# Kernel tuning notes

Hardware: AMD Instinct MI355X
Metric: run time of the kernel (lower is better)

Reference implementation:

```python
import jax, jax.numpy as jnp
import numpy as np

B, C, L = 8, 64, 65536  # batch, channels, flattened H*W
GN_EPS = 1e-5


def setup_inputs() -> dict:
    key = jax.random.key(0)
    ks = jax.random.split(key, 8)
    return {
        "x": jax.random.normal(ks[0], (B, C, L), dtype=jnp.float32),
        "inj0": jax.random.normal(ks[1], (B, C, L), dtype=jnp.float32),
        "inj1": jax.random.normal(ks[2], (B, C, L), dtype=jnp.float32),
        "residual": jax.random.normal(ks[3], (B, C, L), dtype=jnp.float32),
        "gate_w": jax.random.normal(ks[4], (C, C), dtype=jnp.float32) * (1.0 / np.sqrt(C)),
        "gate_b": jax.random.normal(ks[5], (C,), dtype=jnp.float32) * 0.01,
        "fuse_w": jax.random.normal(ks[6], (C, C), dtype=jnp.float32) * (1.0 / np.sqrt(C)),
        "fuse_b": jax.random.normal(ks[7], (C,), dtype=jnp.float32) * 0.01,
        "gn_w": jnp.ones((C,), dtype=jnp.float32),
        "gn_b": jnp.zeros((C,), dtype=jnp.float32),
    }


def _conv1x1(w, b, t):
    # Conv1d with kernel_size=1: [O,C] x [B,C,L] -> [B,O,L]
    return jnp.einsum('oc,bcl->bol', w, t) + b[None, :, None]


def reference(x, inj0, inj1, residual, gate_w, gate_b, fuse_w, fuse_b, gn_w, gn_b):
    # per-injection gate + elementwise multiply, summed over injections
    acc = jnp.zeros_like(x)
    for inj in (inj0, inj1):  # fixed small list of injection features
        acc = acc + x * _conv1x1(gate_w, gate_b, inj + x)
    # fuse conv + residual + ReLU (dropout p=0 -> identity)
    out = jax.nn.relu(_conv1x1(fuse_w, fuse_b, acc) + residual)
    # GroupNorm(num_groups=1): normalize over (C, L) per sample, per-channel affine
    mean = jnp.mean(out, axis=(1, 2), keepdims=True)
    var = jnp.var(out, axis=(1, 2), keepdims=True)
    out = (out - mean) * jax.lax.rsqrt(var + GN_EPS)
    return out * gn_w[None, :, None] + gn_b[None, :, None]
```

## Files before the change

### kernel.cpp

```cpp
#include <hip/hip_runtime.h>
#include <stdint.h>

#define Bv 8
#define Cv 64
#define Lv 65536
#define TPB 512
#define HALF 128
#define COLS 256
#define BLKS_PER_B (Lv / COLS)
#define GRID1 (Bv * BLKS_PER_B)


typedef __attribute__((ext_vector_type(8))) short short8;
typedef __attribute__((ext_vector_type(4))) float f32x4;

#define SSTRIDE 132

__device__ __forceinline__ uint16_t f2bf(float f) {
    uint32_t u = __float_as_uint(f);
    uint32_t r = u + 0x7FFFu + ((u >> 16) & 1u);
    return (uint16_t)(r >> 16);
}
__device__ __forceinline__ uint32_t pack2bf(float lo, float hi) {
    return (uint32_t)f2bf(lo) | ((uint32_t)f2bf(hi) << 16);
}

__global__ void pass1(const float* __restrict__ x, const float* __restrict__ inj0,
                      const float* __restrict__ inj1, const float* __restrict__ resid,
                      const float* __restrict__ gate_w, const float* __restrict__ gate_b,
                      const float* __restrict__ fuse_w, const float* __restrict__ fuse_b,
                      float* __restrict__ out, float* __restrict__ partials)
{
    __shared__ uint32_t s_buf[32 * SSTRIDE];
    __shared__ uint32_t w_lds[2][64][36];
    __shared__ float cinit[2][64];
    __shared__ float wred[16];

    const int tid  = threadIdx.x;
    const int lane = tid & 63;
    const int w    = tid >> 6;
    const int g    = lane >> 4;
    const int ln   = lane & 15;
    const int n    = 16 * w + ln;

    const int b    = blockIdx.x >> 8;
    const int lb   = blockIdx.x & 255;
    const int bCL  = b * (Cv * Lv);

    {
        const int mat = tid >> 8;
        const int m   = (tid >> 2) & 63;
        const int k0  = (tid & 3) << 4;
        const float* wsrc = mat ? fuse_w : gate_w;
        const float4* w4 = reinterpret_cast<const float4*>(wsrc + m * 64 + k0);
        uint32_t* dst = &w_lds[mat][m][k0 >> 1];
        #pragma unroll
        for (int q = 0; q < 4; ++q) {
            const float4 v = w4[q];
            dst[2 * q]     = pack2bf(v.x, v.y);
            dst[2 * q + 1] = pack2bf(v.z, v.w);
        }
        if (tid < 64) {
            cinit[0][tid] = 2.0f * gate_b[tid];
            cinit[1][tid] = fuse_b[tid];
        }
    }

    float lsum = 0.0f, lsq = 0.0f;

    #pragma unroll 1
    for (int h = 0; h < 2; ++h) {
        const int col0 = lb * COLS + h * HALF;

        #pragma unroll
        for (int uu = 0; uu < 2; ++uu) {
            const int u  = tid + uu * TPB;
            const int kp = u >> 5;
            const int c  = (u & 31) << 2;
            const int rA = bCL + (2 * kp) * Lv + col0 + c;
            const int rB = rA + Lv;
            const float4 xA = *reinterpret_cast<const float4*>(x    + rA);
            const float4 aA = *reinterpret_cast<const float4*>(inj0 + rA);
            const float4 bA = *reinterpret_cast<const float4*>(inj1 + rA);
            const float4 xB = *reinterpret_cast<const float4*>(x    + rB);
            const float4 aB = *reinterpret_cast<const float4*>(inj0 + rB);
            const float4 bB = *reinterpret_cast<const float4*>(inj1 + rB);
            uint4 dw;
            dw.x = pack2bf(aA.x + bA.x + 2.0f * xA.x, aB.x + bB.x + 2.0f * xB.x);
            dw.y = pack2bf(aA.y + bA.y + 2.0f * xA.y, aB.y + bB.y + 2.0f * xB.y);
            dw.z = pack2bf(aA.z + bA.z + 2.0f * xA.z, aB.z + bB.z + 2.0f * xB.z);
            dw.w = pack2bf(aA.w + bA.w + 2.0f * xA.w, aB.w + bB.w + 2.0f * xB.w);
            *reinterpret_cast<uint4*>(&s_buf[kp * SSTRIDE + c]) = dw;
        }
        __syncthreads();

        f32x4 D1[4];
        #pragma unroll
        for (int oc = 0; oc < 4; ++oc) {
            const float4 cb = *reinterpret_cast<const float4*>(&cinit[0][16 * oc + 4 * g]);
            D1[oc][0] = cb.x; D1[oc][1] = cb.y; D1[oc][2] = cb.z; D1[oc][3] = cb.w;
        }
        {
            uint4 B0, B1;
            B0.x = s_buf[(4 * g + 0) * SSTRIDE + n];
            B0.y = s_buf[(4 * g + 1) * SSTRIDE + n];
            B0.z = s_buf[(4 * g + 2) * SSTRIDE + n];
            B0.w = s_buf[(4 * g + 3) * SSTRIDE + n];
            B1.x = s_buf[(16 + 4 * g + 0) * SSTRIDE + n];
            B1.y = s_buf[(16 + 4 * g + 1) * SSTRIDE + n];
            B1.z = s_buf[(16 + 4 * g + 2) * SSTRIDE + n];
            B1.w = s_buf[(16 + 4 * g + 3) * SSTRIDE + n];
            #pragma unroll
            for (int oc = 0; oc < 4; ++oc) {
                const int m = ln + 16 * oc;
                const uint4 A0 = *reinterpret_cast<const uint4*>(&w_lds[0][m][4 * g]);
                const uint4 A1 = *reinterpret_cast<const uint4*>(&w_lds[0][m][16 + 4 * g]);
                D1[oc] = __builtin_amdgcn_mfma_f32_16x16x32_bf16(
                    __builtin_bit_cast(short8, A0), __builtin_bit_cast(short8, B0),
                    D1[oc], 0, 0, 0);
                D1[oc] = __builtin_amdgcn_mfma_f32_16x16x32_bf16(
                    __builtin_bit_cast(short8, A1), __builtin_bit_cast(short8, B1),
                    D1[oc], 0, 0, 0);
            }
        }

        {
            const int cg = bCL + col0 + n;
            #pragma unroll
            for (int oc = 0; oc < 4; ++oc) {
                const int m0 = 16 * oc + 4 * g;
                float av[4];
                #pragma unroll
                for (int j = 0; j < 4; ++j)
                    av[j] = x[cg + (m0 + j) * Lv] * D1[oc][j];
                const int kp = 8 * oc + 2 * g;
                s_buf[kp * SSTRIDE + n]       = pack2bf(av[0], av[1]);
                s_buf[(kp + 1) * SSTRIDE + n] = pack2bf(av[2], av[3]);
            }
        }
        __syncthreads();

        f32x4 D2[4];
        #pragma unroll
        for (int oc = 0; oc < 4; ++oc) {
            const float4 cb = *reinterpret_cast<const float4*>(&cinit[1][16 * oc + 4 * g]);
            D2[oc][0] = cb.x; D2[oc][1] = cb.y; D2[oc][2] = cb.z; D2[oc][3] = cb.w;
        }
        {
            uint4 B0, B1;
            B0.x = s_buf[(4 * g + 0) * SSTRIDE + n];
            B0.y = s_buf[(4 * g + 1) * SSTRIDE + n];
            B0.z = s_buf[(4 * g + 2) * SSTRIDE + n];
            B0.w = s_buf[(4 * g + 3) * SSTRIDE + n];
            B1.x = s_buf[(16 + 4 * g + 0) * SSTRIDE + n];
            B1.y = s_buf[(16 + 4 * g + 1) * SSTRIDE + n];
            B1.z = s_buf[(16 + 4 * g + 2) * SSTRIDE + n];
            B1.w = s_buf[(16 + 4 * g + 3) * SSTRIDE + n];
            #pragma unroll
            for (int oc = 0; oc < 4; ++oc) {
                const int m = ln + 16 * oc;
                const uint4 A0 = *reinterpret_cast<const uint4*>(&w_lds[1][m][4 * g]);
                const uint4 A1 = *reinterpret_cast<const uint4*>(&w_lds[1][m][16 + 4 * g]);
                D2[oc] = __builtin_amdgcn_mfma_f32_16x16x32_bf16(
                    __builtin_bit_cast(short8, A0), __builtin_bit_cast(short8, B0),
                    D2[oc], 0, 0, 0);
                D2[oc] = __builtin_amdgcn_mfma_f32_16x16x32_bf16(
                    __builtin_bit_cast(short8, A1), __builtin_bit_cast(short8, B1),
                    D2[oc], 0, 0, 0);
            }
        }
        __syncthreads();

        {
            float* uf = reinterpret_cast<float*>(s_buf);
            const int rowin = tid >> 4;
            const int cl    = tid & 15;
            #pragma unroll 1
            for (int ck = 0; ck < 2; ++ck) {
                #pragma unroll
                for (int oc2 = 0; oc2 < 2; ++oc2) {
                    const int oc = 2 * ck + oc2;
                    #pragma unroll
                    for (int j = 0; j < 4; ++j)
                        uf[(16 * oc2 + 4 * g + j) * SSTRIDE + n] = D2[oc][j];
                }
                const int m   = 32 * ck + rowin;
                const int gbm = bCL + m * Lv + col0;
                const float4 ra = *reinterpret_cast<const float4*>(&resid[gbm + 4 * cl]);
                const float4 rb = *reinterpret_cast<const float4*>(&resid[gbm + 4 * cl + 64]);
                __syncthreads();
                float4 va = *reinterpret_cast<const float4*>(&uf[rowin * SSTRIDE + 4 * cl]);
                float4 vb = *reinterpret_cast<const float4*>(&uf[rowin * SSTRIDE + 4 * cl + 64]);
                va.x = fmaxf(va.x + ra.x, 0.0f); va.y = fmaxf(va.y + ra.y, 0.0f);
                va.z = fmaxf(va.z + ra.z, 0.0f); va.w = fmaxf(va.w + ra.w, 0.0f);
                vb.x = fmaxf(vb.x + rb.x, 0.0f); vb.y = fmaxf(vb.y + rb.y, 0.0f);
                vb.z = fmaxf(vb.z + rb.z, 0.0f); vb.w = fmaxf(vb.w + rb.w, 0.0f);
                *reinterpret_cast<float4*>(&out[gbm + 4 * cl])      = va;
                *reinterpret_cast<float4*>(&out[gbm + 4 * cl + 64]) = vb;
                lsum += (va.x + va.y) + (va.z + va.w) + (vb.x + vb.y) + (vb.z + vb.w);
                lsq = fmaf(va.x, va.x, lsq); lsq = fmaf(va.y, va.y, lsq);
                lsq = fmaf(va.z, va.z, lsq); lsq = fmaf(va.w, va.w, lsq);
                lsq = fmaf(vb.x, vb.x, lsq); lsq = fmaf(vb.y, vb.y, lsq);
                lsq = fmaf(vb.z, vb.z, lsq); lsq = fmaf(vb.w, vb.w, lsq);
                __syncthreads();
            }
        }
    }

    #pragma unroll
    for (int st = 1; st < 64; st <<= 1) {
        lsum += __shfl_xor(lsum, st);
        lsq  += __shfl_xor(lsq,  st);
    }
    if (lane == 0) { wred[2 * w] = lsum; wred[2 * w + 1] = lsq; }
    __syncthreads();
    if (tid == 0) {
        float s = 0.0f, q = 0.0f;
        #pragma unroll
        for (int i = 0; i < 8; ++i) { s += wred[2 * i]; q += wred[2 * i + 1]; }
        partials[2 * blockIdx.x]     = s;
        partials[2 * blockIdx.x + 1] = q;
    }
}

__global__ __launch_bounds__(256)
void pass2(const float* __restrict__ partials, const float* __restrict__ gn_w,
           const float* __restrict__ gn_b, float* __restrict__ sb)
{
    __shared__ float r1[256], r2[256];
    __shared__ float mean_s, rs_s;
    const int b = blockIdx.x, tid = threadIdx.x;
    r1[tid] = partials[2 * (b * 256 + tid)];
    r2[tid] = partials[2 * (b * 256 + tid) + 1];
    __syncthreads();
    #pragma unroll
    for (int st = 128; st > 0; st >>= 1) {
        if (tid < st) { r1[tid] += r1[tid + st]; r2[tid] += r2[tid + st]; }
        __syncthreads();
    }
    if (tid == 0) {
        const float n = (float)Cv * (float)Lv;
        const float mean = r1[0] / n;
        const float var  = r2[0] / n - mean * mean;
        mean_s = mean;
        rs_s   = rsqrtf(var + 1e-5f);
    }
    __syncthreads();
    if (tid < Cv) {
        const float sc = gn_w[tid] * rs_s;
        sb[b * Cv + tid]           = sc;
        sb[Bv * Cv + b * Cv + tid] = fmaf(-mean_s, sc, gn_b[tid]);
    }
}

__global__ __launch_bounds__(256)
void pass3(float* __restrict__ out, const float* __restrict__ sb)
{
    const int total4 = (Bv * Cv * Lv) / 4;
    for (int i = blockIdx.x * blockDim.x + threadIdx.x; i < total4;
         i += gridDim.x * blockDim.x) {
        const int row = i >> 14;
        const float sc = sb[row];
        const float bi = sb[Bv * Cv + row];
        float4 v = reinterpret_cast<float4*>(out)[i];
        v.x = fmaf(v.x, sc, bi);
        v.y = fmaf(v.y, sc, bi);
        v.z = fmaf(v.z, sc, bi);
        v.w = fmaf(v.w, sc, bi);
        reinterpret_cast<float4*>(out)[i] = v;
    }
}

extern "C" void kernel_launch(void* const* d_in, const int* in_sizes, int n_in,
                              void* d_out, int out_size, void* d_ws, size_t ws_size,
                              hipStream_t stream)
{
    const float* x      = (const float*)d_in[0];
    const float* inj0   = (const float*)d_in[1];
    const float* inj1   = (const float*)d_in[2];
    const float* resid  = (const float*)d_in[3];
    const float* gate_w = (const float*)d_in[4];
    const float* gate_b = (const float*)d_in[5];
    const float* fuse_w = (const float*)d_in[6];
    const float* fuse_b = (const float*)d_in[7];
    const float* gn_w   = (const float*)d_in[8];
    const float* gn_b   = (const float*)d_in[9];

    float* out      = (float*)d_out;
    float* ws       = (float*)d_ws;
    float* partials = ws;
    float* sb       = ws + 2 * GRID1;

    hipLaunchKernelGGL(pass1, dim3(GRID1), dim3(TPB), 0, stream,
                       x, inj0, inj1, resid, gate_w, gate_b, fuse_w, fuse_b,
                       out, partials);
    hipLaunchKernelGGL(pass2, dim3(Bv), dim3(256), 0, stream,
                       partials, gn_w, gn_b, sb);
    hipLaunchKernelGGL(pass3, dim3(2048), dim3(256), 0, stream, out, sb);
}
```

Measured before the change: 191.4 us.

## Double-buffer staging LDS and prefetch next half-tile during GEMM

```diff
diff --git a/kernel.cpp b/kernel.cpp
--- a/kernel.cpp
+++ b/kernel.cpp
@@ -31,7 +31,7 @@
                       const float* __restrict__ fuse_w, const float* __restrict__ fuse_b,
                       float* __restrict__ out, float* __restrict__ partials)
 {
-    __shared__ uint32_t s_buf[32 * SSTRIDE];
+    __shared__ uint32_t s_buf[2][32 * SSTRIDE];
     __shared__ uint32_t w_lds[2][64][36];
     __shared__ float cinit[2][64];
     __shared__ float wred[16];
@@ -46,38 +46,15 @@
     const int b    = blockIdx.x >> 8;
     const int lb   = blockIdx.x & 255;
     const int bCL  = b * (Cv * Lv);
-
-    {
-        const int mat = tid >> 8;
-        const int m   = (tid >> 2) & 63;
-        const int k0  = (tid & 3) << 4;
-        const float* wsrc = mat ? fuse_w : gate_w;
-        const float4* w4 = reinterpret_cast<const float4*>(wsrc + m * 64 + k0);
-        uint32_t* dst = &w_lds[mat][m][k0 >> 1];
-        #pragma unroll
-        for (int q = 0; q < 4; ++q) {
-            const float4 v = w4[q];
-            dst[2 * q]     = pack2bf(v.x, v.y);
-            dst[2 * q + 1] = pack2bf(v.z, v.w);
-        }
-        if (tid < 64) {
-            cinit[0][tid] = 2.0f * gate_b[tid];
-            cinit[1][tid] = fuse_b[tid];
-        }
-    }
-
-    float lsum = 0.0f, lsq = 0.0f;
-
-    #pragma unroll 1
-    for (int h = 0; h < 2; ++h) {
-        const int col0 = lb * COLS + h * HALF;
-
+    const int tile0 = lb * COLS;
+
+    auto stage_half = [&](int dst, int scol) {
         #pragma unroll
         for (int uu = 0; uu < 2; ++uu) {
             const int u  = tid + uu * TPB;
             const int kp = u >> 5;
             const int c  = (u & 31) << 2;
-            const int rA = bCL + (2 * kp) * Lv + col0 + c;
+            const int rA = bCL + (2 * kp) * Lv + scol + c;
             const int rB = rA + Lv;
             const float4 xA = *reinterpret_cast<const float4*>(x    + rA);
             const float4 aA = *reinterpret_cast<const float4*>(inj0 + rA);
@@ -90,9 +67,47 @@
             dw.y = pack2bf(aA.y + bA.y + 2.0f * xA.y, aB.y + bB.y + 2.0f * xB.y);
             dw.z = pack2bf(aA.z + bA.z + 2.0f * xA.z, aB.z + bB.z + 2.0f * xB.z);
             dw.w = pack2bf(aA.w + bA.w + 2.0f * xA.w, aB.w + bB.w + 2.0f * xB.w);
-            *reinterpret_cast<uint4*>(&s_buf[kp * SSTRIDE + c]) = dw;
-        }
-        __syncthreads();
+            *reinterpret_cast<uint4*>(&s_buf[dst][kp * SSTRIDE + c]) = dw;
+        }
+    };
+
+    {
+        const int mat = tid >> 8;
+        const int m   = (tid >> 2) & 63;
+        const int k0  = (tid & 3) << 4;
+        const float* wsrc = mat ? fuse_w : gate_w;
+        const float4* w4 = reinterpret_cast<const float4*>(wsrc + m * 64 + k0);
+        uint32_t* dst = &w_lds[mat][m][k0 >> 1];
+        #pragma unroll
+        for (int q = 0; q < 4; ++q) {
+            const float4 v = w4[q];
+            dst[2 * q]     = pack2bf(v.x, v.y);
+            dst[2 * q + 1] = pack2bf(v.z, v.w);
+        }
+        if (tid < 64) {
+            cinit[0][tid] = 2.0f * gate_b[tid];
+            cinit[1][tid] = fuse_b[tid];
+        }
+    }
+    stage_half(0, tile0);
+    __syncthreads();
+
+    float lsum = 0.0f, lsq = 0.0f;
+
+    #pragma unroll 1
+    for (int h = 0; h < 2; ++h) {
+        const int cur  = h;
+        const int col0 = tile0 + h * HALF;
+
+        float xp[16];
+        {
+            const int cg = bCL + col0 + n;
+            #pragma unroll
+            for (int oc = 0; oc < 4; ++oc)
+                #pragma unroll
+                for (int j = 0; j < 4; ++j)
+                    xp[4 * oc + j] = x[cg + (16 * oc + 4 * g + j) * Lv];
+        }
 
         f32x4 D1[4];
         #pragma unroll
@@ -102,14 +117,14 @@
         }
         {
             uint4 B0, B1;
-            B0.x = s_buf[(4 * g + 0) * SSTRIDE + n];
-            B0.y = s_buf[(4 * g + 1) * SSTRIDE + n];
-            B0.z = s_buf[(4 * g + 2) * SSTRIDE + n];
-            B0.w = s_buf[(4 * g + 3) * SSTRIDE + n];
-            B1.x = s_buf[(16 + 4 * g + 0) * SSTRIDE + n];
-            B1.y = s_buf[(16 + 4 * g + 1) * SSTRIDE + n];
-            B1.z = s_buf[(16 + 4 * g + 2) * SSTRIDE + n];
-            B1.w = s_buf[(16 + 4 * g + 3) * SSTRIDE + n];
+            B0.x = s_buf[cur][(4 * g + 0) * SSTRIDE + n];
+            B0.y = s_buf[cur][(4 * g + 1) * SSTRIDE + n];
+            B0.z = s_buf[cur][(4 * g + 2) * SSTRIDE + n];
+            B0.w = s_buf[cur][(4 * g + 3) * SSTRIDE + n];
+            B1.x = s_buf[cur][(16 + 4 * g + 0) * SSTRIDE + n];
+            B1.y = s_buf[cur][(16 + 4 * g + 1) * SSTRIDE + n];
+            B1.z = s_buf[cur][(16 + 4 * g + 2) * SSTRIDE + n];
+            B1.w = s_buf[cur][(16 + 4 * g + 3) * SSTRIDE + n];
             #pragma unroll
             for (int oc = 0; oc < 4; ++oc) {
                 const int m = ln + 16 * oc;
@@ -124,21 +139,18 @@
             }
         }
 
-        {
-            const int cg = bCL + col0 + n;
+        if (h == 0) stage_half(1, tile0 + HALF);
+
+        #pragma unroll
+        for (int oc = 0; oc < 4; ++oc) {
+            float av[4];
             #pragma unroll
-            for (int oc = 0; oc < 4; ++oc) {
-                const int m0 = 16 * oc + 4 * g;
-                float av[4];
-                #pragma unroll
-                for (int j = 0; j < 4; ++j)
-                    av[j] = x[cg + (m0 + j) * Lv] * D1[oc][j];
-                const int kp = 8 * oc + 2 * g;
-                s_buf[kp * SSTRIDE + n]       = pack2bf(av[0], av[1]);
-                s_buf[(kp + 1) * SSTRIDE + n] = pack2bf(av[2], av[3]);
-            }
-        }
-        __syncthreads();
+            for (int j = 0; j < 4; ++j)
+                av[j] = xp[4 * oc + j] * D1[oc][j];
+            const int kp = 8 * oc + 2 * g;
+            s_buf[cur][kp * SSTRIDE + n]       = pack2bf(av[0], av[1]);
+            s_buf[cur][(kp + 1) * SSTRIDE + n] = pack2bf(av[2], av[3]);
+        }
 
         f32x4 D2[4];
         #pragma unroll
@@ -148,14 +160,14 @@
         }
         {
             uint4 B0, B1;
-            B0.x = s_buf[(4 * g + 0) * SSTRIDE + n];
-            B0.y = s_buf[(4 * g + 1) * SSTRIDE + n];
-            B0.z = s_buf[(4 * g + 2) * SSTRIDE + n];
-            B0.w = s_buf[(4 * g + 3) * SSTRIDE + n];
-            B1.x = s_buf[(16 + 4 * g + 0) * SSTRIDE + n];
-            B1.y = s_buf[(16 + 4 * g + 1) * SSTRIDE + n];
-            B1.z = s_buf[(16 + 4 * g + 2) * SSTRIDE + n];
-            B1.w = s_buf[(16 + 4 * g + 3) * SSTRIDE + n];
+            B0.x = s_buf[cur][(4 * g + 0) * SSTRIDE + n];
+            B0.y = s_buf[cur][(4 * g + 1) * SSTRIDE + n];
+            B0.z = s_buf[cur][(4 * g + 2) * SSTRIDE + n];
+            B0.w = s_buf[cur][(4 * g + 3) * SSTRIDE + n];
+            B1.x = s_buf[cur][(16 + 4 * g + 0) * SSTRIDE + n];
+            B1.y = s_buf[cur][(16 + 4 * g + 1) * SSTRIDE + n];
+            B1.z = s_buf[cur][(16 + 4 * g + 2) * SSTRIDE + n];
+            B1.w = s_buf[cur][(16 + 4 * g + 3) * SSTRIDE + n];
             #pragma unroll
             for (int oc = 0; oc < 4; ++oc) {
                 const int m = ln + 16 * oc;
@@ -169,10 +181,9 @@
                     D2[oc], 0, 0, 0);
             }
         }
-        __syncthreads();
 
         {
-            float* uf = reinterpret_cast<float*>(s_buf);
+            float* uf = reinterpret_cast<float*>(s_buf[cur]);
             const int rowin = tid >> 4;
             const int cl    = tid & 15;
             #pragma unroll 1
```

New measurement: 186.6 us. 1.03x faster.
